# Kernel optimization log

Hardware: AMD Instinct MI355X
Metric: run time of the kernel (lower is better)

The kernel has to match this reference:

```python
import jax, jax.numpy as jnp
import numpy as np

H = 8          # n_heads
D_HEAD = 64    # head_dim; scores scaled by sqrt(D_HEAD)


def setup_inputs() -> dict:
    key = jax.random.key(0)
    ks = jax.random.split(key, 9)
    B, S, Dm = 8, 1024, 512
    return {
        "input_Q": jax.random.normal(ks[0], (B, S, Dm), jnp.float32),
        "input_K": jax.random.normal(ks[1], (B, S, Dm), jnp.float32),
        "input_V": jax.random.normal(ks[2], (B, S, Dm), jnp.float32),
        "attn_mask": jax.random.randint(ks[3], (B, S, S), 0, 2).astype(bool),
        "edge_encoding": jax.random.normal(ks[4], (B, S, S), jnp.float32),
        "W_Q": jax.random.normal(ks[5], (Dm, Dm), jnp.float32) / np.sqrt(Dm),
        "W_K": jax.random.normal(ks[6], (Dm, Dm), jnp.float32) / np.sqrt(Dm),
        "W_V": jax.random.normal(ks[7], (Dm, Dm), jnp.float32) / np.sqrt(Dm),
        "W_fc": jax.random.normal(ks[8], (Dm, Dm), jnp.float32) / np.sqrt(Dm),
    }


def reference(input_Q, input_K, input_V, attn_mask, edge_encoding, W_Q, W_K, W_V, W_fc):
    B, S, Dm = input_Q.shape
    # project and split heads: [B, H, S, d_head]
    def heads(x, W):
        return (x @ W).reshape(B, S, H, D_HEAD).transpose(0, 2, 1, 3)
    Q = heads(input_Q, W_Q)
    K = heads(input_K, W_K)
    V = heads(input_V, W_V)
    scores = jnp.einsum("bhqd,bhkd->bhqk", Q, K) / np.sqrt(D_HEAD)
    scores = scores + edge_encoding[:, None, :, :]
    scores = jnp.where(attn_mask[:, None, :, :], jnp.float32(-1e9), scores)
    attn = jax.nn.softmax(scores, axis=-1)
    context = jnp.einsum("bhqk,bhkd->bhqd", attn, V)
    context = context.transpose(0, 2, 1, 3).reshape(B, S, Dm)
    output = context @ W_fc
    scores_avg = scores.sum(axis=1) / H  # [B, S, S]
    return output, scores_avg
```

## Files before the change

kernel.cpp:

```cpp
#include <hip/hip_runtime.h>
#include <math.h>

#define B_ 8
#define S_ 1024
#define DM 512
#define H_ 8
#define DH 64

typedef _Float16 h4 __attribute__((ext_vector_type(4)));
typedef _Float16 h8 __attribute__((ext_vector_type(8)));
typedef float f4 __attribute__((ext_vector_type(4)));

#define MFMA16(a, b, c) __builtin_amdgcn_mfma_f32_16x16x32_f16(a, b, c, 0, 0, 0)

__global__ __launch_bounds__(256) void cast_x(
    const float* __restrict__ x0, const float* __restrict__ x1,
    const float* __restrict__ x2, _Float16* __restrict__ y0,
    _Float16* __restrict__ y1, _Float16* __restrict__ y2) {
  const float* x = (blockIdx.y == 0) ? x0 : (blockIdx.y == 1) ? x1 : x2;
  _Float16* y = (blockIdx.y == 0) ? y0 : (blockIdx.y == 1) ? y1 : y2;
  size_t i = (size_t)blockIdx.x * 1024 + (size_t)threadIdx.x * 4;
  float4 v = *(const float4*)(x + i);
  h4 hv = {(_Float16)v.x, (_Float16)v.y, (_Float16)v.z, (_Float16)v.w};
  *(h4*)(y + i) = hv;
}

__global__ __launch_bounds__(256) void cast_w(
    const float* __restrict__ w0, const float* __restrict__ w1,
    const float* __restrict__ w2, const float* __restrict__ w3,
    _Float16* __restrict__ t0, _Float16* __restrict__ t1,
    _Float16* __restrict__ t2, _Float16* __restrict__ t3) {
  const float* W;
  _Float16* T;
  switch (blockIdx.z) {
    case 0: W = w0; T = t0; break;
    case 1: W = w1; T = t1; break;
    case 2: W = w2; T = t2; break;
    default: W = w3; T = t3; break;
  }
  __shared__ _Float16 ts[64][72];
  const int t = threadIdx.x;
  const int r = t >> 2, c0 = (t & 3) * 16;
  const int n0 = blockIdx.x * 64, k0 = blockIdx.y * 64;
#pragma unroll
  for (int i = 0; i < 4; i++) {
    float4 v = *(const float4*)&W[(size_t)(k0 + r) * 512 + n0 + c0 + i * 4];
    h4 hv = {(_Float16)v.x, (_Float16)v.y, (_Float16)v.z, (_Float16)v.w};
    *(h4*)&ts[r][c0 + i * 4] = hv;
  }
  __syncthreads();
  alignas(16) _Float16 outv[16];
#pragma unroll
  for (int i = 0; i < 16; i++) outv[i] = ts[c0 + i][r];
  *(uint4*)&T[(size_t)(n0 + r) * 512 + k0 + c0] = *(uint4*)&outv[0];
  *(uint4*)&T[(size_t)(n0 + r) * 512 + k0 + c0 + 8] = *(uint4*)&outv[8];
}

__global__ __launch_bounds__(256) void gemm_qkv(
    const _Float16* __restrict__ Xq, const _Float16* __restrict__ Xk,
    const _Float16* __restrict__ Xv, const _Float16* __restrict__ Wt,
    _Float16* __restrict__ Qh, _Float16* __restrict__ Kh,
    _Float16* __restrict__ Vth) {
  const int z = blockIdx.z;
  const int id = blockIdx.x + 4 * blockIdx.y;
  const int c = id & 7, r = id >> 3;
  const int by = c + 8 * (r & 7);
  const int bx = r >> 3;
  const _Float16* A = (z == 0) ? Xq : (z == 1) ? Xk : Xv;
  const _Float16* Bt = Wt + (size_t)z * 512 * 512;
  __shared__ _Float16 Sh[128 * 144];
  const int t = threadIdx.x, lane = t & 63, w = t >> 6;
  const int quad = lane >> 4, l16 = lane & 15;
  const int row0 = by * 128, col0 = bx * 128;
  const int wm = (w & 1) * 64, wn = (w >> 1) * 64;
  f4 acc[4][4] = {};
  const _Float16* Ab = A + (size_t)(row0 + wm + l16) * DM + quad * 8;
  const _Float16* Bb = Bt + (size_t)(col0 + wn + l16) * DM + quad * 8;
#pragma unroll 2
  for (int k0 = 0; k0 < DM; k0 += 64) {
    h8 af[4][2], bf[4][2];
#pragma unroll
    for (int m = 0; m < 4; m++) {
      const _Float16* ap = Ab + (size_t)m * 16 * DM + k0;
      const _Float16* bp = Bb + (size_t)m * 16 * DM + k0;
      af[m][0] = *(const h8*)ap;
      af[m][1] = *(const h8*)(ap + 32);
      bf[m][0] = *(const h8*)bp;
      bf[m][1] = *(const h8*)(bp + 32);
    }
#pragma unroll
    for (int m = 0; m < 4; m++)
#pragma unroll
      for (int n = 0; n < 4; n++) {
        acc[m][n] = MFMA16(af[m][0], bf[n][0], acc[m][n]);
        acc[m][n] = MFMA16(af[m][1], bf[n][1], acc[m][n]);
      }
  }
  if (z < 2) {
    _Float16* C = (z == 0) ? Qh : Kh;
#pragma unroll
    for (int m = 0; m < 4; m++)
#pragma unroll
      for (int n = 0; n < 4; n++)
#pragma unroll
        for (int reg = 0; reg < 4; reg++)
          Sh[(wm + m * 16 + quad * 4 + reg) * 144 + wn + n * 16 + l16] =
              (_Float16)acc[m][n][reg];
    __syncthreads();
    const int rr = t >> 4;
    const int cs = (t & 15) * 8;
#pragma unroll
    for (int i = 0; i < 8; i++) {
      int row = rr + 16 * i;
      *(uint4*)&C[(size_t)(row0 + row) * DM + col0 + cs] =
          *(uint4*)&Sh[row * 144 + cs];
    }
  } else {
#pragma unroll
    for (int m = 0; m < 4; m++)
#pragma unroll
      for (int n = 0; n < 4; n++) {
        h4 vv = {(_Float16)acc[m][n][0], (_Float16)acc[m][n][1],
                 (_Float16)acc[m][n][2], (_Float16)acc[m][n][3]};
        *(h4*)&Sh[(wn + n * 16 + l16) * 144 + wm + m * 16 + quad * 4] = vv;
      }
    __syncthreads();
    const int rr = t >> 4;
    const int cs = (t & 15) * 8;
    const int b = row0 >> 10, s0 = row0 & 1023;
#pragma unroll
    for (int i = 0; i < 8; i++) {
      int cg = col0 + rr + 16 * i;
      int h = cg >> 6, d = cg & 63;
      *(uint4*)&Vth[((size_t)(b * 8 + h) * 64 + d) * S_ + s0 + cs] =
          *(uint4*)&Sh[(rr + 16 * i) * 144 + cs];
    }
  }
}

__global__ __launch_bounds__(256) void gemm_fc(
    const _Float16* __restrict__ A, const _Float16* __restrict__ Bt,
    float* __restrict__ C) {
  const int id = blockIdx.x + 4 * blockIdx.y;
  const int c = id & 7, r = id >> 3;
  const int by = c + 8 * (r & 15);
  const int bx = r >> 4;
  const int t = threadIdx.x, lane = t & 63, w = t >> 6;
  const int quad = lane >> 4, l16 = lane & 15;
  const int row0 = by * 64, col0 = bx * 128;
  const int wm = (w & 1) * 32, wn = (w >> 1) * 64;
  f4 acc[2][4] = {};
  const _Float16* Ab = A + (size_t)(row0 + wm + l16) * DM + quad * 8;
  const _Float16* Bb = Bt + (size_t)(col0 + wn + l16) * DM + quad * 8;
#pragma unroll 2
  for (int k0 = 0; k0 < DM; k0 += 64) {
    h8 af[2][2], bf[4][2];
#pragma unroll
    for (int m = 0; m < 2; m++) {
      const _Float16* ap = Ab + (size_t)m * 16 * DM + k0;
      af[m][0] = *(const h8*)ap;
      af[m][1] = *(const h8*)(ap + 32);
    }
#pragma unroll
    for (int n = 0; n < 4; n++) {
      const _Float16* bp = Bb + (size_t)n * 16 * DM + k0;
      bf[n][0] = *(const h8*)bp;
      bf[n][1] = *(const h8*)(bp + 32);
    }
#pragma unroll
    for (int m = 0; m < 2; m++)
#pragma unroll
      for (int n = 0; n < 4; n++) {
        acc[m][n] = MFMA16(af[m][0], bf[n][0], acc[m][n]);
        acc[m][n] = MFMA16(af[m][1], bf[n][1], acc[m][n]);
      }
  }
#pragma unroll
  for (int m = 0; m < 2; m++)
#pragma unroll
    for (int n = 0; n < 4; n++)
#pragma unroll
      for (int reg = 0; reg < 4; reg++) {
        size_t row = row0 + wm + m * 16 + quad * 4 + reg;
        size_t col = col0 + wn + n * 16 + l16;
        C[row * DM + col] = acc[m][n][reg];
      }
}

__global__ __launch_bounds__(256) void scores_mfma(
    const _Float16* __restrict__ Qh, const _Float16* __restrict__ Kh,
    const int* __restrict__ mask, const float* __restrict__ edge,
    float* __restrict__ out1, _Float16* __restrict__ Ehs) {
  const int b = blockIdx.z;
  const int id = blockIdx.x + 8 * blockIdx.y;
  const int iy = id & 7, jx = id >> 3;
  const int i0 = iy * 128, j0 = jx * 128;
  const _Float16* A = Qh + (size_t)b * S_ * DM;
  const _Float16* Bt = Kh + (size_t)b * S_ * DM;
  const int t = threadIdx.x, lane = t & 63, w = t >> 6;
  const int quad = lane >> 4, l16 = lane & 15;
  const int wm = (w & 1) * 64, wn = (w >> 1) * 64;
  f4 acc[4][4] = {};
  const _Float16* Ab = A + (size_t)(i0 + wm + l16) * DM + quad * 8;
  const _Float16* Bb = Bt + (size_t)(j0 + wn + l16) * DM + quad * 8;
#pragma unroll 2
  for (int k0 = 0; k0 < DM; k0 += 64) {
    h8 af[4][2], bf[4][2];
#pragma unroll
    for (int m = 0; m < 4; m++) {
      const _Float16* ap = Ab + (size_t)m * 16 * DM + k0;
      const _Float16* bp = Bb + (size_t)m * 16 * DM + k0;
      af[m][0] = *(const h8*)ap;
      af[m][1] = *(const h8*)(ap + 32);
      bf[m][0] = *(const h8*)bp;
      bf[m][1] = *(const h8*)(bp + 32);
    }
#pragma unroll
    for (int m = 0; m < 4; m++)
#pragma unroll
      for (int n = 0; n < 4; n++) {
        acc[m][n] = MFMA16(bf[n][0], af[m][0], acc[m][n]);
        acc[m][n] = MFMA16(bf[n][1], af[m][1], acc[m][n]);
      }
  }
  const int jt = (j0 + wn) >> 6;
#pragma unroll
  for (int m = 0; m < 4; m++) {
    size_t gi = i0 + wm + m * 16 + l16;
    size_t rowb = ((size_t)b * S_ + gi) * S_;
    const size_t qg = (size_t)(i0 + wm + m * 16) >> 4;
    const size_t ehb = (((size_t)b * 16 + jt) * 64 + qg) * 16;
#pragma unroll
    for (int n = 0; n < 4; n++) {
      int jloc = n * 16 + quad * 4;
      size_t idx = rowb + j0 + wn + jloc;
      int4 mk4 = *(const int4*)&mask[idx];
      float4 e4 = *(const float4*)&edge[idx];
      float o[4];
      h4 ev;
      const int mk[4] = {mk4.x, mk4.y, mk4.z, mk4.w};
      const float ee[4] = {e4.x, e4.y, e4.z, e4.w};
#pragma unroll
      for (int reg = 0; reg < 4; reg++) {
        o[reg] = mk[reg] ? -1e9f : (acc[m][n][reg] * (1.0f / 64.0f) + ee[reg]);
        ev[reg] = mk[reg] ? (_Float16)(-65504.0f) : (_Float16)(ee[reg] - 8.0f);
      }
      *(float4*)&out1[idx] = make_float4(o[0], o[1], o[2], o[3]);
      *(h4*)&Ehs[(ehb + n * 4 + quad) * 64 + l16 * 4] = ev;
    }
  }
}

__global__ __launch_bounds__(256, 2) void flash_mfma(
    const _Float16* __restrict__ Qh, const _Float16* __restrict__ Kh,
    const _Float16* __restrict__ Vth, const _Float16* __restrict__ Ehs,
    _Float16* __restrict__ ctxh) {
  __shared__ _Float16 Ps[128][72], Ks[64][72], Vt[64][72];
  const int t = threadIdx.x, lane = t & 63, w = t >> 6;
  const int quad = lane >> 4, l16 = lane & 15;
  const int g = blockIdx.x + 8 * blockIdx.y;
  const int c = g & 7, r = g >> 3;
  const int bh = c + 8 * (r & 7);
  const int qb = r >> 3;
  const int b = bh >> 3, h = bh & 7;
  const int q0 = qb * 128;
  const size_t bS = (size_t)b * S_;
  const int sr = t >> 3, sc = (t & 7) * 8;
  const int qw = w * 32;
  const size_t qg0 = (size_t)(q0 + qw) >> 4;

#pragma unroll
  for (int i = 0; i < 4; i++)
    *(uint4*)&Ps[sr + 32 * i][sc] =
        *(const uint4*)&Qh[(bS + q0 + sr + 32 * i) * DM + h * DH + sc];
  __syncthreads();
  h8 aq[2][2];
#pragma unroll
  for (int m = 0; m < 2; m++)
#pragma unroll
    for (int k = 0; k < 2; k++)
      aq[m][k] = *(h8*)&Ps[qw + m * 16 + l16][k * 32 + quad * 8];

  uint4 kv[4];
  kv[0] = *(const uint4*)&Kh[(bS + sr) * DM + h * DH + sc];
  kv[1] = *(const uint4*)&Kh[(bS + sr + 32) * DM + h * DH + sc];
  kv[2] = *(const uint4*)&Vth[((size_t)bh * 64 + sr) * S_ + sc];
  kv[3] = *(const uint4*)&Vth[((size_t)bh * 64 + sr + 32) * S_ + sc];
  h4 evh[2][4];
#pragma unroll
  for (int m = 0; m < 2; m++) {
    const size_t ehb = (((size_t)b * 16 + 0) * 64 + qg0 + m) * 16;
#pragma unroll
    for (int n = 0; n < 4; n++)
      evh[m][n] = *(const h4*)&Ehs[(ehb + n * 4 + quad) * 64 + l16 * 4];
  }

  f4 acco[2][4] = {};
  f4 accl[2] = {};

  h8 vone;
#pragma unroll
  for (int i = 0; i < 8; i++) vone[i] = (_Float16)1.0f;

  for (int kb = 0; kb < S_; kb += 64) {
    __syncthreads();
    *(uint4*)&Ks[sr][sc] = kv[0];
    *(uint4*)&Ks[sr + 32][sc] = kv[1];
    *(uint4*)&Vt[sr][sc] = kv[2];
    *(uint4*)&Vt[sr + 32][sc] = kv[3];
    __syncthreads();
    const int kn = kb + 64;
    h4 evn[2][4];
    if (kn < S_) {
      kv[0] = *(const uint4*)&Kh[(bS + kn + sr) * DM + h * DH + sc];
      kv[1] = *(const uint4*)&Kh[(bS + kn + sr + 32) * DM + h * DH + sc];
      kv[2] = *(const uint4*)&Vth[((size_t)bh * 64 + sr) * S_ + kn + sc];
      kv[3] = *(const uint4*)&Vth[((size_t)bh * 64 + sr + 32) * S_ + kn + sc];
#pragma unroll
      for (int m = 0; m < 2; m++) {
        const size_t ehb = (((size_t)b * 16 + (kn >> 6)) * 64 + qg0 + m) * 16;
#pragma unroll
        for (int n = 0; n < 4; n++)
          evn[m][n] = *(const h4*)&Ehs[(ehb + n * 4 + quad) * 64 + l16 * 4];
      }
    }
    f4 accs[2][4] = {};
#pragma unroll
    for (int n = 0; n < 4; n++) {
      h8 b0 = *(h8*)&Ks[n * 16 + l16][quad * 8];
      h8 b1 = *(h8*)&Ks[n * 16 + l16][32 + quad * 8];
#pragma unroll
      for (int m = 0; m < 2; m++) {
        accs[m][n] = MFMA16(b0, aq[m][0], accs[m][n]);
        accs[m][n] = MFMA16(b1, aq[m][1], accs[m][n]);
      }
    }
#pragma unroll
    for (int m = 0; m < 2; m++)
#pragma unroll
      for (int n = 0; n < 4; n++) {
        h4 pv;
#pragma unroll
        for (int reg = 0; reg < 4; reg++)
          pv[reg] = (_Float16)__expf(accs[m][n][reg] * 0.125f +
                                     (float)evh[m][n][reg]);
        *(h4*)&Ps[qw + m * 16 + l16][n * 16 + quad * 4] = pv;
      }
    h8 ap[2][2];
#pragma unroll
    for (int m = 0; m < 2; m++)
#pragma unroll
      for (int k = 0; k < 2; k++)
        ap[m][k] = *(h8*)&Ps[qw + m * 16 + l16][k * 32 + quad * 8];
#pragma unroll
    for (int d = 0; d < 4; d++) {
      h8 bv0 = *(h8*)&Vt[d * 16 + l16][quad * 8];
      h8 bv1 = *(h8*)&Vt[d * 16 + l16][32 + quad * 8];
#pragma unroll
      for (int m = 0; m < 2; m++) {
        acco[m][d] = MFMA16(ap[m][0], bv0, acco[m][d]);
        acco[m][d] = MFMA16(ap[m][1], bv1, acco[m][d]);
      }
    }
#pragma unroll
    for (int m = 0; m < 2; m++) {
      accl[m] = MFMA16(ap[m][0], vone, accl[m]);
      accl[m] = MFMA16(ap[m][1], vone, accl[m]);
    }
    if (kn < S_) {
#pragma unroll
      for (int m = 0; m < 2; m++)
#pragma unroll
        for (int n = 0; n < 4; n++) evh[m][n] = evn[m][n];
    }
  }
#pragma unroll
  for (int m = 0; m < 2; m++)
#pragma unroll
    for (int d = 0; d < 4; d++)
#pragma unroll
      for (int reg = 0; reg < 4; reg++)
        Ps[qw + m * 16 + quad * 4 + reg][d * 16 + l16] =
            (_Float16)(acco[m][d][reg] / accl[m][reg]);
  __syncthreads();
  const int orr = t >> 3, ocs = (t & 7) * 8;
#pragma unroll
  for (int i = 0; i < 4; i++) {
    int row = orr + 32 * i;
    *(uint4*)&ctxh[(bS + q0 + row) * DM + h * DH + ocs] =
        *(uint4*)&Ps[row][ocs];
  }
}

extern "C" void kernel_launch(void* const* d_in, const int* in_sizes, int n_in,
                              void* d_out, int out_size, void* d_ws,
                              size_t ws_size, hipStream_t stream) {
  const float* Xq = (const float*)d_in[0];
  const float* Xk = (const float*)d_in[1];
  const float* Xv = (const float*)d_in[2];
  const int* mask = (const int*)d_in[3];
  const float* edge = (const float*)d_in[4];
  const float* Wq = (const float*)d_in[5];
  const float* Wk = (const float*)d_in[6];
  const float* Wv = (const float*)d_in[7];
  const float* Wfc = (const float*)d_in[8];

  float* out0 = (float*)d_out;
  float* out1 = out0 + (size_t)B_ * S_ * DM;

  const size_t NE = (size_t)B_ * S_ * DM;
  char* ws = (char*)d_ws;
  _Float16* Qh = (_Float16*)ws;
  _Float16* Kh = Qh + NE;
  _Float16* Vth = Kh + NE;
  _Float16* Xhq = Vth + NE;
  _Float16* Xhk = Xhq + NE;
  _Float16* Xhv = Xhk + NE;
  _Float16* Wt = Xhv + NE;
  _Float16* Wtf = Wt + 3 * 512 * 512;
  _Float16* Ehs = Wt + 4 * 512 * 512;
  _Float16* ctxh = Xhq;

  dim3 blk(256);
  cast_x<<<dim3(4096, 3), blk, 0, stream>>>(Xq, Xk, Xv, Xhq, Xhk, Xhv);
  cast_w<<<dim3(8, 8, 4), blk, 0, stream>>>(Wq, Wk, Wv, Wfc, Wt,
                                            Wt + 512 * 512, Wt + 2 * 512 * 512,
                                            Wtf);
  gemm_qkv<<<dim3(4, 64, 3), blk, 0, stream>>>(Xhq, Xhk, Xhv, Wt, Qh, Kh, Vth);
  scores_mfma<<<dim3(8, 8, 8), blk, 0, stream>>>(Qh, Kh, mask, edge, out1,
                                                 Ehs);
  flash_mfma<<<dim3(8, 64), blk, 0, stream>>>(Qh, Kh, Vth, Ehs, ctxh);
  gemm_fc<<<dim3(4, 128), blk, 0, stream>>>(ctxh, Wtf, out0);
}
```

Before: 348.4 us.

## Double-buffer K/V tiles in LDS to halve per-iteration barriers

The K and V shared-memory tiles become ping-pong buffers. The next tile is written into the alternate buffer while the current one is consumed, and global loads are prefetched two tiles ahead. This cuts the loop from two __syncthreads per iteration to one and overlaps the LDS stores with compute. In exchange it needs more LDS per block (roughly 18KB extra), which may reduce occupancy, and holds the prefetched data in registers for longer.

```diff
diff --git a/kernel.cpp b/kernel.cpp
--- a/kernel.cpp
+++ b/kernel.cpp
@@ -255,7 +255,8 @@
     const _Float16* __restrict__ Qh, const _Float16* __restrict__ Kh,
     const _Float16* __restrict__ Vth, const _Float16* __restrict__ Ehs,
     _Float16* __restrict__ ctxh) {
-  __shared__ _Float16 Ps[128][72], Ks[64][72], Vt[64][72];
+  __shared__ _Float16 Ps[128][72];
+  __shared__ _Float16 Ks[2][64][72], Vt[2][64][72];
   const int t = threadIdx.x, lane = t & 63, w = t >> 6;
   const int quad = lane >> 4, l16 = lane & 15;
   const int g = blockIdx.x + 8 * blockIdx.y;
@@ -273,19 +274,29 @@
   for (int i = 0; i < 4; i++)
     *(uint4*)&Ps[sr + 32 * i][sc] =
         *(const uint4*)&Qh[(bS + q0 + sr + 32 * i) * DM + h * DH + sc];
-  __syncthreads();
-  h8 aq[2][2];
-#pragma unroll
-  for (int m = 0; m < 2; m++)
-#pragma unroll
-    for (int k = 0; k < 2; k++)
-      aq[m][k] = *(h8*)&Ps[qw + m * 16 + l16][k * 32 + quad * 8];
 
   uint4 kv[4];
   kv[0] = *(const uint4*)&Kh[(bS + sr) * DM + h * DH + sc];
   kv[1] = *(const uint4*)&Kh[(bS + sr + 32) * DM + h * DH + sc];
   kv[2] = *(const uint4*)&Vth[((size_t)bh * 64 + sr) * S_ + sc];
   kv[3] = *(const uint4*)&Vth[((size_t)bh * 64 + sr + 32) * S_ + sc];
+  *(uint4*)&Ks[0][sr][sc] = kv[0];
+  *(uint4*)&Ks[0][sr + 32][sc] = kv[1];
+  *(uint4*)&Vt[0][sr][sc] = kv[2];
+  *(uint4*)&Vt[0][sr + 32][sc] = kv[3];
+  __syncthreads();
+
+  h8 aq[2][2];
+#pragma unroll
+  for (int m = 0; m < 2; m++)
+#pragma unroll
+    for (int k = 0; k < 2; k++)
+      aq[m][k] = *(h8*)&Ps[qw + m * 16 + l16][k * 32 + quad * 8];
+
+  kv[0] = *(const uint4*)&Kh[(bS + 64 + sr) * DM + h * DH + sc];
+  kv[1] = *(const uint4*)&Kh[(bS + 64 + sr + 32) * DM + h * DH + sc];
+  kv[2] = *(const uint4*)&Vth[((size_t)bh * 64 + sr) * S_ + 64 + sc];
+  kv[3] = *(const uint4*)&Vth[((size_t)bh * 64 + sr + 32) * S_ + 64 + sc];
   h4 evh[2][4];
 #pragma unroll
   for (int m = 0; m < 2; m++) {
@@ -303,19 +314,24 @@
   for (int i = 0; i < 8; i++) vone[i] = (_Float16)1.0f;
 
   for (int kb = 0; kb < S_; kb += 64) {
-    __syncthreads();
-    *(uint4*)&Ks[sr][sc] = kv[0];
-    *(uint4*)&Ks[sr + 32][sc] = kv[1];
-    *(uint4*)&Vt[sr][sc] = kv[2];
-    *(uint4*)&Vt[sr + 32][sc] = kv[3];
-    __syncthreads();
+    const int cur = (kb >> 6) & 1;
+    const int nxt = cur ^ 1;
     const int kn = kb + 64;
+    if (kn < S_) {
+      *(uint4*)&Ks[nxt][sr][sc] = kv[0];
+      *(uint4*)&Ks[nxt][sr + 32][sc] = kv[1];
+      *(uint4*)&Vt[nxt][sr][sc] = kv[2];
+      *(uint4*)&Vt[nxt][sr + 32][sc] = kv[3];
+    }
+    if (kn + 64 < S_) {
+      kv[0] = *(const uint4*)&Kh[(bS + kn + 64 + sr) * DM + h * DH + sc];
+      kv[1] = *(const uint4*)&Kh[(bS + kn + 64 + sr + 32) * DM + h * DH + sc];
+      kv[2] = *(const uint4*)&Vth[((size_t)bh * 64 + sr) * S_ + kn + 64 + sc];
+      kv[3] =
+          *(const uint4*)&Vth[((size_t)bh * 64 + sr + 32) * S_ + kn + 64 + sc];
+    }
     h4 evn[2][4];
     if (kn < S_) {
-      kv[0] = *(const uint4*)&Kh[(bS + kn + sr) * DM + h * DH + sc];
-      kv[1] = *(const uint4*)&Kh[(bS + kn + sr + 32) * DM + h * DH + sc];
-      kv[2] = *(const uint4*)&Vth[((size_t)bh * 64 + sr) * S_ + kn + sc];
-      kv[3] = *(const uint4*)&Vth[((size_t)bh * 64 + sr + 32) * S_ + kn + sc];
 #pragma unroll
       for (int m = 0; m < 2; m++) {
         const size_t ehb = (((size_t)b * 16 + (kn >> 6)) * 64 + qg0 + m) * 16;
@@ -327,8 +343,8 @@
     f4 accs[2][4] = {};
 #pragma unroll
     for (int n = 0; n < 4; n++) {
-      h8 b0 = *(h8*)&Ks[n * 16 + l16][quad * 8];
-      h8 b1 = *(h8*)&Ks[n * 16 + l16][32 + quad * 8];
+      h8 b0 = *(h8*)&Ks[cur][n * 16 + l16][quad * 8];
+      h8 b1 = *(h8*)&Ks[cur][n * 16 + l16][32 + quad * 8];
 #pragma unroll
       for (int m = 0; m < 2; m++) {
         accs[m][n] = MFMA16(b0, aq[m][0], accs[m][n]);
@@ -354,8 +370,8 @@
         ap[m][k] = *(h8*)&Ps[qw + m * 16 + l16][k * 32 + quad * 8];
 #pragma unroll
     for (int d = 0; d < 4; d++) {
-      h8 bv0 = *(h8*)&Vt[d * 16 + l16][quad * 8];
-      h8 bv1 = *(h8*)&Vt[d * 16 + l16][32 + quad * 8];
+      h8 bv0 = *(h8*)&Vt[cur][d * 16 + l16][quad * 8];
+      h8 bv1 = *(h8*)&Vt[cur][d * 16 + l16][32 + quad * 8];
 #pragma unroll
       for (int m = 0; m < 2; m++) {
         acco[m][d] = MFMA16(ap[m][0], bv0, acco[m][d]);
@@ -373,6 +389,7 @@
 #pragma unroll
         for (int n = 0; n < 4; n++) evh[m][n] = evn[m][n];
     }
+    __syncthreads();
   }
 #pragma unroll
   for (int m = 0; m < 2; m++)
```

New measurement: 347.7 us. About the same (-0.2%).
